# Performance work log

Measured on AMD Instinct MI355X. Metric: run time of the kernel, lower is better.

The kernel has to match this reference:

```python
import jax, jax.numpy as jnp
import numpy as np

NUM_HEADS = 16
HEAD_DIM = 64
TOP_K_TILES = 8
TILE_SIZE = 16
ROPE_BASE = 10000.0


def make_freqs_cis(seq_len, head_dim):
    # [seq, head_dim//2] complex64, standard RoPE frequencies
    inv_freq = 1.0 / (ROPE_BASE ** (jnp.arange(0, head_dim, 2, dtype=jnp.float32) / head_dim))
    angles = jnp.arange(seq_len, dtype=jnp.float32)[:, None] * inv_freq[None, :]
    return jax.lax.complex(jnp.cos(angles), jnp.sin(angles))


def apply_rope(xq, xk, freqs_cis):
    # xq, xk: [b, h, s, d]; pairs adjacent channels as (real, imag)
    xq_ = xq.astype(jnp.float32).reshape(*xq.shape[:-1], -1, 2)
    xk_ = xk.astype(jnp.float32).reshape(*xk.shape[:-1], -1, 2)
    xq_c = jax.lax.complex(xq_[..., 0], xq_[..., 1])
    xk_c = jax.lax.complex(xk_[..., 0], xk_[..., 1])
    f = freqs_cis[None, None, :xq.shape[2], :]
    xq_r = xq_c * f
    xk_r = xk_c * f
    xq_out = jnp.stack([xq_r.real, xq_r.imag], axis=-1).reshape(xq.shape)
    xk_out = jnp.stack([xk_r.real, xk_r.imag], axis=-1).reshape(xk.shape)
    return xq_out.astype(xq.dtype), xk_out.astype(xk.dtype)


def setup_inputs() -> dict:
    key = jax.random.key(0)
    ks = jax.random.split(key, 5)
    B, S, D = 2, 2048, 1024
    scale = 1.0 / np.sqrt(D)
    return {
        "x": jax.random.normal(ks[0], (B, S, D), dtype=jnp.float32),
        "wq": jax.random.normal(ks[1], (D, NUM_HEADS * HEAD_DIM), dtype=jnp.float32) * scale,
        "wk": jax.random.normal(ks[2], (D, NUM_HEADS * HEAD_DIM), dtype=jnp.float32) * scale,
        "wv": jax.random.normal(ks[3], (D, NUM_HEADS * HEAD_DIM), dtype=jnp.float32) * scale,
        "wo": jax.random.normal(ks[4], (NUM_HEADS * HEAD_DIM, D), dtype=jnp.float32) * scale,
    }


def reference(x, wq, wk, wv, wo):
    batch, seq_len, _ = x.shape
    q = (x @ wq).reshape(batch, seq_len, NUM_HEADS, HEAD_DIM)
    k = (x @ wk).reshape(batch, seq_len, NUM_HEADS, HEAD_DIM)
    v = (x @ wv).reshape(batch, seq_len, NUM_HEADS, HEAD_DIM)

    freqs_cis = make_freqs_cis(seq_len, HEAD_DIM)
    q_t = jnp.transpose(q, (0, 2, 1, 3))
    k_t = jnp.transpose(k, (0, 2, 1, 3))
    q_t, k_t = apply_rope(q_t, k_t, freqs_cis)
    q = jnp.transpose(q_t, (0, 2, 1, 3))
    k = jnp.transpose(k_t, (0, 2, 1, 3))

    logits = jnp.einsum('bqhd,bkhd->bhqk', q, k) / jnp.sqrt(jnp.float32(HEAD_DIM))
    causal = jnp.tril(jnp.ones((seq_len, seq_len), dtype=bool))
    logits = jnp.where(causal[None, None, :, :], logits, -1e10)
    weights = jax.nn.softmax(logits, axis=-1)  # [b, h, q, k]

    # Scout: tile-max-pool last token's attention probs + top-k tile selection
    last_token_probs = weights[:, :, -1, :]  # [b, h, k]
    pad_len = (TILE_SIZE - seq_len % TILE_SIZE) % TILE_SIZE
    if pad_len > 0:
        last_token_probs = jnp.pad(last_token_probs, ((0, 0), (0, 0), (0, pad_len)))
    num_tiles = last_token_probs.shape[-1] // TILE_SIZE
    tile_scores = jnp.max(
        last_token_probs.reshape(batch, NUM_HEADS, num_tiles, TILE_SIZE), axis=-1)
    _, top_tile_indices = jax.lax.top_k(tile_scores, TOP_K_TILES)  # [b, h, top_k]

    output = jnp.einsum('bhqk,bkhd->bqhd', weights, v)
    output = output.reshape(batch, seq_len, NUM_HEADS * HEAD_DIM)
    output = output @ wo
    return output, top_tile_indices
```

## Files before the change

kernel.cpp:

```cpp
#include <hip/hip_runtime.h>

#define B_ 2
#define S_ 2048
#define E_ 1024
#define H_ 16
#define D_ 64
#define BS_ (B_*S_)
#define PSTR 76

typedef unsigned short u16;
typedef __attribute__((ext_vector_type(8))) short short8;
typedef __attribute__((ext_vector_type(4))) float floatx4;
typedef __bf16 bf16x8 __attribute__((ext_vector_type(8)));

__device__ __forceinline__ u16 f2bf(float f) {
    unsigned int u = __builtin_bit_cast(unsigned int, f);
    u += 0x7FFFu + ((u >> 16) & 1u);
    return (u16)(u >> 16);
}
__device__ __forceinline__ float bf2f(u16 h) {
    return __builtin_bit_cast(float, (unsigned int)h << 16);
}
__device__ __forceinline__ floatx4 mfma16(short8 a, short8 b, floatx4 c) {
    return __builtin_amdgcn_mfma_f32_16x16x32_bf16(
        __builtin_bit_cast(bf16x8, a), __builtin_bit_cast(bf16x8, b), c, 0, 0, 0);
}
__device__ __forceinline__ void gload_lds16(const void* g, void* l) {
    __builtin_amdgcn_global_load_lds(
        (const __attribute__((address_space(1))) unsigned int*)g,
        (__attribute__((address_space(3))) unsigned int*)l, 16, 0, 0);
}

__global__ __launch_bounds__(256) void prep_kernel(const float* __restrict__ x,
                                                   const float* __restrict__ wq,
                                                   const float* __restrict__ wk,
                                                   const float* __restrict__ wv,
                                                   const float* __restrict__ wo,
                                                   u16* __restrict__ xcat,
                                                   u16* __restrict__ wqt,
                                                   u16* __restrict__ wkt,
                                                   u16* __restrict__ wkres,
                                                   u16* __restrict__ wvt,
                                                   u16* __restrict__ wot,
                                                   float* __restrict__ cost,
                                                   float* __restrict__ sint,
                                                   float* __restrict__ qlast) {
    __shared__ float t[32][33];
    int bx = blockIdx.x;
    int tid = threadIdx.x;
    if (bx < 4096) {
        int i = bx * 256 + tid;
        int row = i >> 8, c4 = (i & 255) * 4;
        float4 v = ((const float4*)x)[i];
        u16 h0 = f2bf(v.x), h1 = f2bf(v.y), h2 = f2bf(v.z), h3 = f2bf(v.w);
        uint2 o;
        o.x = (unsigned)h0 | ((unsigned)h1 << 16);
        o.y = (unsigned)h2 | ((unsigned)h3 << 16);
        *(uint2*)&xcat[(size_t)row * 2048 + c4] = o;
        u16 l0 = f2bf(v.x - bf2f(h0)), l1 = f2bf(v.y - bf2f(h1));
        u16 l2 = f2bf(v.z - bf2f(h2)), l3 = f2bf(v.w - bf2f(h3));
        uint2 ol;
        ol.x = (unsigned)l0 | ((unsigned)l1 << 16);
        ol.y = (unsigned)l2 | ((unsigned)l3 << 16);
        *(uint2*)&xcat[(size_t)row * 2048 + 1024 + c4] = ol;
    } else if (bx < 8192) {
        int sub = bx - 4096;
        int which = sub >> 10, s2 = sub & 1023;
        const float* W = which == 0 ? wq : which == 1 ? wk : which == 2 ? wv : wo;
        u16* Wt = which == 0 ? wqt : which == 1 ? wkt : which == 2 ? wvt : wot;
        int tk = (s2 >> 5) * 32, tn = (s2 & 31) * 32;
        int tx = tid & 31, ty = tid >> 5;
        for (int i = 0; i < 32; i += 8)
            t[ty + i][tx] = W[(size_t)(tk + ty + i) * E_ + tn + tx];
        __syncthreads();
        for (int i = 0; i < 32; i += 8) {
            float v = t[tx][ty + i];
            u16 hi = f2bf(v);
            Wt[(size_t)(tn + ty + i) * E_ + tk + tx] = hi;
            if (which == 1) {
                wkres[(size_t)(tn + ty + i) * 2048 + tk + tx] = f2bf(v - bf2f(hi));
                wkres[(size_t)(tn + ty + i) * 2048 + 1024 + tk + tx] = hi;
            }
        }
    } else if (bx < 8448) {
        int idx = (bx - 8192) * 256 + tid;
        int s = idx >> 5, i = idx & 31;
        float inv = powf(10000.0f, -(float)i / 32.0f);
        float a = (float)s * inv;
        cost[idx] = cosf(a);
        sint[idx] = sinf(a);
    } else {
        float* red = &t[0][0];
        int b2 = bx - 8448;
        int b = b2 >> 5, c0 = (b2 & 31) * 32;
        int cl = tid & 31, kc = tid >> 5;
        const float* xr = &x[((size_t)b * S_ + (S_ - 1)) * E_ + kc * 128];
        const float* wp = &wq[(size_t)(kc * 128) * E_ + c0 + cl];
        float acc = 0.f;
#pragma unroll 4
        for (int e = 0; e < 128; ++e) acc = fmaf(xr[e], wp[(size_t)e * E_], acc);
        red[kc * 32 + cl] = acc;
        __syncthreads();
        if (kc == 0) {
            float s = ((red[0 * 32 + cl] + red[1 * 32 + cl]) + (red[2 * 32 + cl] + red[3 * 32 + cl]))
                    + ((red[4 * 32 + cl] + red[5 * 32 + cl]) + (red[6 * 32 + cl] + red[7 * 32 + cl]));
            qlast[(size_t)b * E_ + c0 + cl] = s;
        }
    }
}


__device__ __forceinline__ void stage_swz(const u16* __restrict__ src, int row0, int k0,
                                          int stride, u16* lds, int tid) {
    int wv = tid >> 6, ln = tid & 63;
    int swz = (((ln & 7) ^ (ln >> 3)) << 3);
    int rr = ln >> 3;
#pragma unroll
    for (int i = 0; i < 4; ++i) {
        int seg = i * 4 + wv;
        gload_lds16(&src[(size_t)(row0 + seg * 8 + rr) * stride + k0 + swz],
                    (char*)lds + (size_t)seg * 1024);
    }
}

__device__ __forceinline__ void gemm_body(const u16* lA, const u16* lB,
                                          floatx4 (*acc)[4], int lane, int wave) {
    int wm = (wave >> 1) * 64, wn = (wave & 1) * 64;
    int lr = lane & 15, lq = lane >> 4, r7 = lr & 7;
#pragma unroll
    for (int half = 0; half < 2; ++half) {
        int xo = (((half * 4 + lq) ^ r7) << 3);
        short8 afr[4], bfr[4];
#pragma unroll
        for (int mi = 0; mi < 4; ++mi)
            afr[mi] = *(const short8*)&lA[(wm + mi * 16 + lr) * 64 + xo];
#pragma unroll
        for (int ni = 0; ni < 4; ++ni)
            bfr[ni] = *(const short8*)&lB[(wn + ni * 16 + lr) * 64 + xo];
        __builtin_amdgcn_s_setprio(1);
#pragma unroll
        for (int mi = 0; mi < 4; ++mi)
#pragma unroll
            for (int ni = 0; ni < 4; ++ni)
                acc[mi][ni] = mfma16(afr[mi], bfr[ni], acc[mi][ni]);
        __builtin_amdgcn_s_setprio(0);
    }
}

__device__ __forceinline__ void gemm_write(float* __restrict__ C, floatx4 (*acc)[4],
                                           int m0, int n0, int N, int lane, int wave) {
    int wm = (wave >> 1) * 64, wn = (wave & 1) * 64;
    int lr = lane & 15, lq = lane >> 4;
#pragma unroll
    for (int mi = 0; mi < 4; ++mi)
#pragma unroll
        for (int ni = 0; ni < 4; ++ni)
#pragma unroll
            for (int r = 0; r < 4; ++r)
                C[(size_t)(m0 + wm + mi * 16 + lq * 4 + r) * N + n0 + wn + ni * 16 + lr]
                    = acc[mi][ni][r];
}

__device__ __forceinline__ void rope_epilogue(floatx4 (*acc)[4], int m0, int n0,
                                              const float* __restrict__ cost,
                                              const float* __restrict__ sint,
                                              const float* __restrict__ qlast,
                                              u16* __restrict__ dstb,
                                              float* __restrict__ tscores,
                                              int lane, int wave) {
    int wm = (wave >> 1) * 64, wn = (wave & 1) * 64;
    int lr = lane & 15, lq = lane >> 4;
    int odd = lr & 1;
    int h = (n0 + wn) >> 6;
    int bq = m0 >> 11;
    int s0 = m0 & 2047;
    float qr[4];
    if (qlast) {
#pragma unroll
        for (int ni = 0; ni < 4; ++ni) {
            int d = ni * 16 + lr;
            int i = d >> 1;
            float qv = qlast[(size_t)bq * E_ + h * 64 + d];
            float qp = __shfl_xor(qv, 1);
            float c = cost[2047 * 32 + i], sn = sint[2047 * 32 + i];
            qr[ni] = odd ? (qp * sn + qv * c) : (qv * c - qp * sn);
        }
    }
    float dotp[4][4];
#pragma unroll
    for (int mi = 0; mi < 4; ++mi)
#pragma unroll
        for (int r = 0; r < 4; ++r) dotp[mi][r] = 0.f;
#pragma unroll
    for (int ni = 0; ni < 4; ++ni) {
        int d = ni * 16 + lr;
        int i = d >> 1;
#pragma unroll
        for (int mi = 0; mi < 4; ++mi) {
#pragma unroll
            for (int r = 0; r < 4; ++r) {
                int row = m0 + wm + mi * 16 + lq * 4 + r;
                int s = row & 2047;
                float own = acc[mi][ni][r];
                float par = __shfl_xor(own, 1);
                float c = cost[s * 32 + i], sn = sint[s * 32 + i];
                float out = odd ? (par * sn + own * c) : (own * c - par * sn);
                dstb[(((size_t)(bq * 16 + h)) * S_ + s) * 64 + d] = f2bf(out);
                if (qlast) dotp[mi][r] += out * qr[ni];
            }
        }
    }
    if (qlast) {
#pragma unroll
        for (int mi = 0; mi < 4; ++mi) {
            float tm = -1e30f;
#pragma unroll
            for (int r = 0; r < 4; ++r) {
                float dv = dotp[mi][r];
                dv += __shfl_xor(dv, 1);
                dv += __shfl_xor(dv, 2);
                dv += __shfl_xor(dv, 4);
                dv += __shfl_xor(dv, 8);
                tm = fmaxf(tm, dv);
            }
            tm = fmaxf(tm, __shfl_xor(tm, 16));
            tm = fmaxf(tm, __shfl_xor(tm, 32));
            if (lane == 0)
                tscores[(size_t)(bq * 16 + h) * 128 + (s0 >> 4) + (wm >> 4) + mi] = tm;
        }
    }
}

__device__ __forceinline__ void v_epilogue(floatx4 (*acc)[4], int m0, int n0,
                                           u16* vt, u16* __restrict__ vtb,
                                           int lane, int wave, int tid) {
    int wm = (wave >> 1) * 64, wn = (wave & 1) * 64;
    int lr = lane & 15, lq = lane >> 4;
#pragma unroll
    for (int ni = 0; ni < 4; ++ni) {
        int dcol = wn + ni * 16 + lr;
#pragma unroll
        for (int mi = 0; mi < 4; ++mi)
#pragma unroll
            for (int r = 0; r < 4; ++r)
                vt[dcol * 136 + wm + mi * 16 + lq * 4 + r] = f2bf(acc[mi][ni][r]);
    }
    __syncthreads();
    int dcol = tid >> 1, sh = (tid & 1) * 64;
    int colg = n0 + dcol, h = colg >> 6, d = colg & 63;
    int bq = m0 >> 11, s0 = m0 & 2047;
    size_t base = (((size_t)(bq * 16 + h)) * 64 + d) * S_ + s0 + sh;
#pragma unroll
    for (int c = 0; c < 8; ++c)
        *(uint4*)&vtb[base + c * 8] = *(const uint4*)&vt[dcol * 136 + sh + c * 8];
}

__global__ __launch_bounds__(256) void proj_gemm_kernel(const u16* __restrict__ xcat,
                                                        const u16* __restrict__ wqt,
                                                        const u16* __restrict__ wkt,
                                                        const u16* __restrict__ wkres,
                                                        const u16* __restrict__ wvt,
                                                        const float* __restrict__ cost,
                                                        const float* __restrict__ sint,
                                                        const float* __restrict__ qlast,
                                                        u16* __restrict__ qb,
                                                        u16* __restrict__ kb,
                                                        float* __restrict__ tscores,
                                                        u16* __restrict__ vtb) {
    __shared__ __align__(16) u16 lds4[4 * 8192];
    u16* T0 = lds4;
    u16* T1 = lds4 + 8192;
    u16* T2 = lds4 + 16384;
    u16* T3 = lds4 + 24576;
    int bx = blockIdx.x;
    int role = bx >> 8;
    int idx = bx & 255;
    int xcd = idx & 7, loc = idx >> 3;
    int m0 = (xcd * 4 + (loc & 3)) * 128;
    int n0 = (loc >> 2) * 128;
    int tid = threadIdx.x, lane = tid & 63, wave = tid >> 6;

    floatx4 acc[4][4];
#pragma unroll
    for (int i = 0; i < 4; ++i)
#pragma unroll
        for (int j = 0; j < 4; ++j) acc[i][j] = (floatx4){0.f, 0.f, 0.f, 0.f};

    if (role == 0) {
        for (int k0 = 0; k0 < 1024; k0 += 64) {
            stage_swz(xcat, m0, k0, 2048, T0, tid);
            stage_swz(xcat, m0, k0 + 1024, 2048, T1, tid);
            stage_swz(wkt, n0, k0, 1024, T2, tid);
            stage_swz(wkres, n0, k0, 2048, T3, tid);
            asm volatile("s_waitcnt vmcnt(0)" ::: "memory");
            __syncthreads();
            gemm_body(T0, T2, acc, lane, wave);
            gemm_body(T0, T3, acc, lane, wave);
            gemm_body(T1, T2, acc, lane, wave);
            __syncthreads();
        }
        rope_epilogue(acc, m0, n0, cost, sint, qlast, kb, tscores, lane, wave);
    } else {
        const u16* Bt = (role == 1) ? wqt : wvt;
        stage_swz(xcat, m0, 0, 2048, T0, tid);
        stage_swz(Bt, n0, 0, 1024, T2, tid);
        asm volatile("s_waitcnt vmcnt(0)" ::: "memory");
        __syncthreads();
        for (int step = 0; step < 16; ++step) {
            int buf = step & 1;
            u16* Ac = buf ? T1 : T0;
            u16* Bc = buf ? T3 : T2;
            if (step < 15) {
                stage_swz(xcat, m0, (step + 1) * 64, 2048, buf ? T0 : T1, tid);
                stage_swz(Bt, n0, (step + 1) * 64, 1024, buf ? T2 : T3, tid);
            }
            gemm_body(Ac, Bc, acc, lane, wave);
            asm volatile("s_waitcnt vmcnt(0)" ::: "memory");
            __syncthreads();
        }
        if (role == 1)
            rope_epilogue(acc, m0, n0, cost, sint, (const float*)nullptr, qb,
                          (float*)nullptr, lane, wave);
        else
            v_epilogue(acc, m0, n0, lds4, vtb, lane, wave, tid);
    }
}

__global__ __launch_bounds__(256) void gemm_bf16_kernel(const u16* __restrict__ A,
                                                        const u16* __restrict__ Bt,
                                                        float* __restrict__ C,
                                                        int M, int N, int Kd) {
    __shared__ __align__(16) u16 lds4[4 * 8192];
    u16* T0 = lds4;
    u16* T1 = lds4 + 8192;
    u16* T2 = lds4 + 16384;
    u16* T3 = lds4 + 24576;
    int nwg = (M / 128) * (N / 128);
    int bx = blockIdx.x;
    int q = nwg >> 3, rr = nwg & 7, xcd = bx & 7, pos = bx >> 3;
    int lbx = (xcd < rr ? xcd * (q + 1) : rr * (q + 1) + (xcd - rr) * q) + pos;
    int nbn = N / 128;
    int m0 = (lbx / nbn) * 128, n0 = (lbx % nbn) * 128;
    int tid = threadIdx.x, lane = tid & 63, wave = tid >> 6;

    floatx4 acc[4][4];
#pragma unroll
    for (int i = 0; i < 4; ++i)
#pragma unroll
        for (int j = 0; j < 4; ++j) acc[i][j] = (floatx4){0.f, 0.f, 0.f, 0.f};

    int nsteps = Kd / 64;
    stage_swz(A, m0, 0, Kd, T0, tid);
    stage_swz(Bt, n0, 0, Kd, T2, tid);
    asm volatile("s_waitcnt vmcnt(0)" ::: "memory");
    __syncthreads();
    for (int step = 0; step < nsteps; ++step) {
        int buf = step & 1;
        u16* Ac = buf ? T1 : T0;
        u16* Bc = buf ? T3 : T2;
        if (step + 1 < nsteps) {
            stage_swz(A, m0, (step + 1) * 64, Kd, buf ? T0 : T1, tid);
            stage_swz(Bt, n0, (step + 1) * 64, Kd, buf ? T2 : T3, tid);
        }
        gemm_body(Ac, Bc, acc, lane, wave);
        asm volatile("s_waitcnt vmcnt(0)" ::: "memory");
        __syncthreads();
    }
    gemm_write(C, acc, m0, n0, N, lane, wave);
}

__device__ __forceinline__ void stage_kv(const u16* __restrict__ K, const u16* __restrict__ V,
                                         int n0, u16* kbuf, u16* vbuf, int wave, int lane) {
    int lr = lane & 15, lq = lane >> 4;
    if (wave < 2) {
#pragma unroll
        for (int i = 0; i < 4; ++i) {
            int sk = wave * 4 + i;
            int kt = sk >> 1, kh = (sk & 1) * 32;
            gload_lds16(&K[(size_t)(n0 + kt * 16 + lr) * D_ + kh + lq * 8],
                        kbuf + sk * 512);
        }
    } else {
#pragma unroll
        for (int i = 0; i < 4; ++i) {
            int sv = (wave - 2) * 4 + i;
            int c = sv >> 2, o = sv & 3;
            gload_lds16(&V[(size_t)(o * 16 + lr) * S_ + n0 + c * 32 + lq * 8],
                        vbuf + sv * 512);
        }
    }
}

__global__ __launch_bounds__(256) void flash_kernel(const u16* __restrict__ qb,
                                                    const u16* __restrict__ kb,
                                                    const u16* __restrict__ vtb,
                                                    u16* __restrict__ ab) {
    __shared__ __align__(16) u16 kls[2][8 * 512];
    __shared__ __align__(16) u16 vls[2][8 * 512];
    __shared__ __align__(16) u16 ldsP[4][16 * PSTR];
    int tid = threadIdx.x;
    int lane = tid & 63, wave = tid >> 6;
    int bx = blockIdx.x;
    int xcd = bx & 7, ii = bx >> 3;
    int hid = xcd + 8 * (ii & 3);
    int qc = 31 - (ii >> 2);
    int qt0 = qc * 64 + wave * 16;
    const u16* Q = qb + (size_t)hid * S_ * D_;
    const u16* K = kb + (size_t)hid * S_ * D_;
    const u16* V = vtb + (size_t)hid * D_ * S_;
    u16* lp = &ldsP[wave][0];
    int lr = lane & 15, lq = lane >> 4, lk = lq * 8;

    short8 qfr0 = *(const short8*)&Q[(size_t)(qt0 + lr) * D_ + lk];
    short8 qfr1 = *(const short8*)&Q[(size_t)(qt0 + lr) * D_ + 32 + lk];

    floatx4 o0 = {0,0,0,0}, o1 = {0,0,0,0}, o2 = {0,0,0,0}, o3 = {0,0,0,0};
    float m = -1e30f, l = 0.f;

    stage_kv(K, V, 0, kls[0], vls[0], wave, lane);
    asm volatile("s_waitcnt vmcnt(0)" ::: "memory");
    __syncthreads();

    for (int it = 0; it <= qc; ++it) {
        int n0 = it * 64;
        int buf = it & 1;
        const u16* kbuf = kls[buf];
        const u16* vbuf = vls[buf];
        if (it < qc)
            stage_kv(K, V, n0 + 64, kls[buf ^ 1], vls[buf ^ 1], wave, lane);

        short8 ka0[4], ka1[4];
#pragma unroll
        for (int kt = 0; kt < 4; ++kt) {
            ka0[kt] = *(const short8*)&kbuf[(kt * 2 + 0) * 512 + lane * 8];
            ka1[kt] = *(const short8*)&kbuf[(kt * 2 + 1) * 512 + lane * 8];
        }
        floatx4 st[4];
#pragma unroll
        for (int kt = 0; kt < 4; ++kt) st[kt] = (floatx4){0.f, 0.f, 0.f, 0.f};
        __builtin_amdgcn_s_setprio(1);
#pragma unroll
        for (int kt = 0; kt < 4; ++kt) {
            st[kt] = mfma16(ka0[kt], qfr0, st[kt]);
            st[kt] = mfma16(ka1[kt], qfr1, st[kt]);
        }
        __builtin_amdgcn_s_setprio(0);

        const float SC = 0.18033688011112042f;
        int rem = qt0 + 16 - n0;
        float sv[4][4];
        float bmax = -1e30f;
        if (rem >= 80) {
#pragma unroll
            for (int kt = 0; kt < 4; ++kt)
#pragma unroll
                for (int r = 0; r < 4; ++r) {
                    float s = st[kt][r] * SC;
                    sv[kt][r] = s;
                    bmax = fmaxf(bmax, s);
                }
        } else {
#pragma unroll
            for (int kt = 0; kt < 4; ++kt)
#pragma unroll
                for (int r = 0; r < 4; ++r) {
                    int k = n0 + kt * 16 + lq * 4 + r;
                    float s = (k <= qt0 + lr) ? st[kt][r] * SC : -1e30f;
                    sv[kt][r] = s;
                    bmax = fmaxf(bmax, s);
                }
        }
        bmax = fmaxf(bmax, __shfl_xor(bmax, 16));
        bmax = fmaxf(bmax, __shfl_xor(bmax, 32));
        if (!__all(bmax <= m + 8.0f)) {
            float mn = fmaxf(m, bmax);
            float alpha = __builtin_amdgcn_exp2f(m - mn);
            m = mn;
            l *= alpha;
            float af[4];
#pragma unroll
            for (int r = 0; r < 4; ++r) af[r] = __shfl(alpha, lq * 4 + r);
#pragma unroll
            for (int r = 0; r < 4; ++r) {
                o0[r] *= af[r]; o1[r] *= af[r]; o2[r] *= af[r]; o3[r] *= af[r];
            }
        }
        float ps = 0.f;
#pragma unroll
        for (int kt = 0; kt < 4; ++kt) {
            float p0 = __builtin_amdgcn_exp2f(sv[kt][0] - m);
            float p1 = __builtin_amdgcn_exp2f(sv[kt][1] - m);
            float p2 = __builtin_amdgcn_exp2f(sv[kt][2] - m);
            float p3 = __builtin_amdgcn_exp2f(sv[kt][3] - m);
            ps += (p0 + p1) + (p2 + p3);
            unsigned wlo, whi;
            asm("v_cvt_pk_bf16_f32 %0, %1, %2" : "=v"(wlo) : "v"(p0), "v"(p1));
            asm("v_cvt_pk_bf16_f32 %0, %1, %2" : "=v"(whi) : "v"(p2), "v"(p3));
            *(uint2*)&lp[lr * PSTR + kt * 16 + lq * 4] = (uint2){wlo, whi};
        }
        ps += __shfl_xor(ps, 16);
        ps += __shfl_xor(ps, 32);
        l += ps;

        short8 vv[2][4];
#pragma unroll
        for (int c = 0; c < 2; ++c)
#pragma unroll
            for (int o = 0; o < 4; ++o)
                vv[c][o] = *(const short8*)&vbuf[(c * 4 + o) * 512 + lane * 8];
        asm volatile("s_waitcnt lgkmcnt(0)" ::: "memory");
        __builtin_amdgcn_s_setprio(1);
#pragma unroll
        for (int c = 0; c < 2; ++c) {
            uint2 plo = *(const uint2*)&lp[lr * PSTR + c * 32 + lk];
            uint2 phi = *(const uint2*)&lp[lr * PSTR + c * 32 + lk + 4];
            short8 pfr = __builtin_bit_cast(short8, (uint4){plo.x, plo.y, phi.x, phi.y});
            o0 = mfma16(pfr, vv[c][0], o0);
            o1 = mfma16(pfr, vv[c][1], o1);
            o2 = mfma16(pfr, vv[c][2], o2);
            o3 = mfma16(pfr, vv[c][3], o3);
        }
        __builtin_amdgcn_s_setprio(0);

        if (it < qc) {
            asm volatile("s_waitcnt vmcnt(0)" ::: "memory");
            __syncthreads();
        }
    }
    float li[4];
#pragma unroll
    for (int r = 0; r < 4; ++r) li[r] = 1.0f / __shfl(l, lq * 4 + r);
    int b = hid >> 4, h = hid & 15;
    size_t orow_base = ((size_t)b * S_ + qt0 + lq * 4) * E_ + h * D_;
#pragma unroll
    for (int r = 0; r < 4; ++r) {
        size_t rb = orow_base + (size_t)r * E_;
        ab[rb + 0  + lr] = f2bf(o0[r] * li[r]);
        ab[rb + 16 + lr] = f2bf(o1[r] * li[r]);
        ab[rb + 32 + lr] = f2bf(o2[r] * li[r]);
        ab[rb + 48 + lr] = f2bf(o3[r] * li[r]);
    }
}

__global__ __launch_bounds__(64) void topk_select_kernel(const float* __restrict__ tscores,
                                                         float* __restrict__ oidx) {
    int bh = blockIdx.x, tid = threadIdx.x;
    float v0 = tscores[bh * 128 + tid], v1 = tscores[bh * 128 + 64 + tid];
    float va, vb; int ia, ib;
    if (v1 > v0) { va = v1; ia = tid + 64; vb = v0; ib = tid; }
    else         { va = v0; ia = tid;      vb = v1; ib = tid + 64; }
    float cv = va; int ci = ia; int used = 0;
    for (int t = 0; t < 8; ++t) {
        float bv = cv; int bi = ci;
#pragma unroll
        for (int mk = 1; mk < 64; mk <<= 1) {
            float ov = __shfl_xor(bv, mk);
            int oi = __shfl_xor(bi, mk);
            if (ov > bv || (ov == bv && oi < bi)) { bv = ov; bi = oi; }
        }
        if (tid == 0) oidx[bh * 8 + t] = (float)bi;
        if (ci == bi) {
            if (used == 0) { cv = vb; ci = ib; used = 1; }
            else           { cv = -3e30f; ci = 1 << 20; }
        }
    }
}

extern "C" void kernel_launch(void* const* d_in, const int* in_sizes, int n_in,
                              void* d_out, int out_size, void* d_ws, size_t ws_size,
                              hipStream_t stream) {
    (void)in_sizes; (void)n_in; (void)out_size; (void)ws_size;
    const float* x  = (const float*)d_in[0];
    const float* wq = (const float*)d_in[1];
    const float* wk = (const float*)d_in[2];
    const float* wv = (const float*)d_in[3];
    const float* wo = (const float*)d_in[4];
    float* out = (float*)d_out;

    char* wsp = (char*)d_ws;
    size_t off = 0;
    auto nxt = [&](size_t bytes) {
        char* p = wsp + off;
        off = (off + bytes + 255) & ~(size_t)255;
        return p;
    };
    u16* xcat  = (u16*)nxt((size_t)BS_ * 2048 * 2);
    u16* wqt   = (u16*)nxt((size_t)E_ * E_ * 2);
    u16* wkt   = (u16*)nxt((size_t)E_ * E_ * 2);
    u16* wkres = (u16*)nxt((size_t)E_ * 2048 * 2);
    u16* wvt   = (u16*)nxt((size_t)E_ * E_ * 2);
    u16* wot   = (u16*)nxt((size_t)E_ * E_ * 2);
    float* cost = (float*)nxt((size_t)S_ * 32 * 4);
    float* sint = (float*)nxt((size_t)S_ * 32 * 4);
    u16* qb    = (u16*)nxt((size_t)B_ * H_ * S_ * D_ * 2);
    u16* kb    = (u16*)nxt((size_t)B_ * H_ * S_ * D_ * 2);
    u16* vtb   = (u16*)nxt((size_t)B_ * H_ * S_ * D_ * 2);
    u16* ab    = (u16*)nxt((size_t)BS_ * E_ * 2);
    float* qlast = (float*)nxt((size_t)B_ * E_ * 4);
    float* tscores = (float*)nxt((size_t)B_ * H_ * 128 * 4);

    hipLaunchKernelGGL(prep_kernel, dim3(8512), dim3(256), 0, stream,
                       x, wq, wk, wv, wo, xcat, wqt, wkt, wkres, wvt, wot,
                       cost, sint, qlast);

    hipLaunchKernelGGL(proj_gemm_kernel, dim3(768), dim3(256), 0, stream,
                       xcat, wqt, wkt, wkres, wvt, cost, sint, qlast,
                       qb, kb, tscores, vtb);

    hipLaunchKernelGGL(flash_kernel, dim3(B_ * H_ * (S_ / 64)), dim3(256), 0, stream,
                       qb, kb, vtb, ab);

    hipLaunchKernelGGL(topk_select_kernel, dim3(B_ * H_), dim3(64), 0, stream,
                       tscores, out + (size_t)BS_ * E_);

    hipLaunchKernelGGL(gemm_bf16_kernel, dim3(256), dim3(256), 0, stream, ab, wot, out,
                       BS_, E_, E_);
}
```

Baseline: 221.8 us.

## Shrink projection-kernel LDS and drop double-buffering to raise occupancy

Cuts the projection GEMM's shared memory from four 8192-element tiles to one A and one B tile plus epilogue scratch, and replaces the double-buffered pipeline with a simple single-buffered stage/sync/compute loop. The K role now runs two sequential loops (the 1024-wide wkt pass and the 2048-wide wkres pass) instead of three fused gemm_body calls per step. The aim is more resident workgroups per CU so other waves hide load latency. The cost is losing explicit prefetch overlap and re-staging the A tile for the residual pass. The explicit vmcnt waits are also gone, so correctness now depends on stage_swz or __syncthreads ordering the global-to-LDS copies.

Result: faster. 211.5 us (-4.6%).

```diff
diff --git a/kernel.cpp b/kernel.cpp
--- a/kernel.cpp
+++ b/kernel.cpp
@@ -267,11 +267,9 @@
                                                         u16* __restrict__ kb,
                                                         float* __restrict__ tscores,
                                                         u16* __restrict__ vtb) {
-    __shared__ __align__(16) u16 lds4[4 * 8192];
-    u16* T0 = lds4;
-    u16* T1 = lds4 + 8192;
-    u16* T2 = lds4 + 16384;
-    u16* T3 = lds4 + 24576;
+    __shared__ __align__(16) u16 lsbuf[17408];
+    u16* lA = lsbuf;
+    u16* lB = lsbuf + 8192;
     int bx = blockIdx.x;
     int role = bx >> 8;
     int idx = bx & 255;
@@ -288,41 +286,39 @@
 
     if (role == 0) {
         for (int k0 = 0; k0 < 1024; k0 += 64) {
-            stage_swz(xcat, m0, k0, 2048, T0, tid);
-            stage_swz(xcat, m0, k0 + 1024, 2048, T1, tid);
-            stage_swz(wkt, n0, k0, 1024, T2, tid);
-            stage_swz(wkres, n0, k0, 2048, T3, tid);
-            asm volatile("s_waitcnt vmcnt(0)" ::: "memory");
-            __syncthreads();
-            gemm_body(T0, T2, acc, lane, wave);
-            gemm_body(T0, T3, acc, lane, wave);
-            gemm_body(T1, T2, acc, lane, wave);
+            stage_swz(xcat, m0, k0, 2048, lA, tid);
+            stage_swz(wkt, n0, k0, 1024, lB, tid);
+            __syncthreads();
+            gemm_body(lA, lB, acc, lane, wave);
+            __syncthreads();
+        }
+        for (int k0 = 0; k0 < 2048; k0 += 64) {
+            stage_swz(xcat, m0, k0, 2048, lA, tid);
+            stage_swz(wkres, n0, k0, 2048, lB, tid);
+            __syncthreads();
+            gemm_body(lA, lB, acc, lane, wave);
             __syncthreads();
         }
         rope_epilogue(acc, m0, n0, cost, sint, qlast, kb, tscores, lane, wave);
+    } else if (role == 1) {
+        for (int k0 = 0; k0 < 1024; k0 += 64) {
+            stage_swz(xcat, m0, k0, 2048, lA, tid);
+            stage_swz(wqt, n0, k0, 1024, lB, tid);
+            __syncthreads();
+            gemm_body(lA, lB, acc, lane, wave);
+            __syncthreads();
+        }
+        rope_epilogue(acc, m0, n0, cost, sint, (const float*)nullptr, qb,
+                      (float*)nullptr, lane, wave);
     } else {
-        const u16* Bt = (role == 1) ? wqt : wvt;
-        stage_swz(xcat, m0, 0, 2048, T0, tid);
-        stage_swz(Bt, n0, 0, 1024, T2, tid);
-        asm volatile("s_waitcnt vmcnt(0)" ::: "memory");
-        __syncthreads();
-        for (int step = 0; step < 16; ++step) {
-            int buf = step & 1;
-            u16* Ac = buf ? T1 : T0;
-            u16* Bc = buf ? T3 : T2;
-            if (step < 15) {
-                stage_swz(xcat, m0, (step + 1) * 64, 2048, buf ? T0 : T1, tid);
-                stage_swz(Bt, n0, (step + 1) * 64, 1024, buf ? T2 : T3, tid);
-            }
-            gemm_body(Ac, Bc, acc, lane, wave);
-            asm volatile("s_waitcnt vmcnt(0)" ::: "memory");
-            __syncthreads();
-        }
-        if (role == 1)
-            rope_epilogue(acc, m0, n0, cost, sint, (const float*)nullptr, qb,
-                          (float*)nullptr, lane, wave);
-        else
-            v_epilogue(acc, m0, n0, lds4, vtb, lane, wave, tid);
+        for (int k0 = 0; k0 < 1024; k0 += 64) {
+            stage_swz(xcat, m0, k0, 2048, lA, tid);
+            stage_swz(wvt, n0, k0, 1024, lB, tid);
+            __syncthreads();
+            gemm_body(lA, lB, acc, lane, wave);
+            __syncthreads();
+        }
+        v_epilogue(acc, m0, n0, lsbuf, vtb, lane, wave, tid);
     }
 }
 
```
